# Performance work log

Hardware: AMD Instinct MI355X
Metric: run time of the kernel (lower is better)

## Reference

```python
import jax, jax.numpy as jnp
import numpy as np

N_NODES = 50000


def gcn_conv(x, src, dst, W, b, n):
    # PyG GCNConv: h = x @ W; out[i] = sum_j norm_ij * h[j] + b, with added self-loops
    h = x @ W  # [N, out]
    deg = jax.ops.segment_sum(jnp.ones_like(dst, dtype=h.dtype), dst, num_segments=n)
    inv_sqrt_deg = jnp.where(deg > 0, jax.lax.rsqrt(deg), 0.0)  # [N]
    coeff = inv_sqrt_deg[src] * inv_sqrt_deg[dst]  # [E]
    msg = h[src] * coeff[:, None]  # [E, out] gather (memory-bound)
    out = jax.ops.segment_sum(msg, dst, num_segments=n)  # scatter-add
    return out + b


def setup_inputs() -> dict:
    key = jax.random.key(0)
    ks = jax.random.split(key, 8)
    n, e, c_in, c_hid, c_out = N_NODES, 800000, 128, 128, 64
    x = jax.random.normal(ks[0], (n, c_in), dtype=jnp.float32)
    edge_index = jax.random.randint(ks[1], (2, e), 0, n, dtype=jnp.int64)
    # Glorot-ish scaled weights
    W1 = jax.random.normal(ks[2], (c_in, c_hid), dtype=jnp.float32) / np.sqrt(c_in)
    b1 = jnp.zeros((c_hid,), dtype=jnp.float32)
    W2 = jax.random.normal(ks[3], (c_hid, c_out), dtype=jnp.float32) / np.sqrt(c_hid)
    b2 = jnp.zeros((c_out,), dtype=jnp.float32)
    lin_W = jax.random.normal(ks[4], (2 * c_out, c_out), dtype=jnp.float32) / np.sqrt(2 * c_out)
    lin_b = jnp.zeros((c_out,), dtype=jnp.float32)
    return {"x": x, "edge_index": edge_index, "W1": W1, "b1": b1,
            "W2": W2, "b2": b2, "lin_W": lin_W, "lin_b": lin_b}


def reference(x, edge_index, W1, b1, W2, b2, lin_W, lin_b):
    n = x.shape[0]
    # add self-loops (as GCNConv does by default)
    loops = jnp.arange(n, dtype=edge_index.dtype)
    src = jnp.concatenate([edge_index[0], loops])
    dst = jnp.concatenate([edge_index[1], loops])

    def branch(x):
        h = jax.nn.relu(gcn_conv(x, src, dst, W1, b1, n))
        # dropout: identity in eval mode (training=False)
        return gcn_conv(h, src, dst, W2, b2, n)

    x1 = branch(x)
    x2 = branch(x)
    # FusionMethod == 'Concat'
    fused = jnp.concatenate([x1, x2], axis=1) @ lin_W + lin_b
    return jax.nn.log_softmax(fused, axis=1)
```

## Files before the change

kernel.cpp:

```cpp
#include <hip/hip_runtime.h>


#define CIN  128
#define CHID 128
#define COUT 64
#define BCAP_SH 13
#define BCAP    (1 << BCAP_SH)
#define BINCHUNK 2048

typedef short v8s __attribute__((ext_vector_type(8)));
typedef float v4f __attribute__((ext_vector_type(4)));

static __device__ __forceinline__ unsigned short f2bf(float f) {
    unsigned int u = __float_as_uint(f);
    unsigned int r = (u + 0x7fffu + ((u >> 16) & 1u)) >> 16;
    return (unsigned short)r;
}
static __device__ __forceinline__ float bf2f(unsigned short v) {
    return __uint_as_float(((unsigned int)v) << 16);
}

__global__ __launch_bounds__(256) void bin_kernel(const int* __restrict__ src,
                                                  const int* __restrict__ dst,
                                                  int* __restrict__ bcursor,
                                                  unsigned int* __restrict__ binned, int E) {
    __shared__ int h[256];
    __shared__ int base[256];
    int t = threadIdx.x;
    h[t] = 0;
    __syncthreads();
    int e0 = blockIdx.x * BINCHUNK;
    int e1 = e0 + BINCHUNK; if (e1 > E) e1 = E;
    for (int e = e0 + t; e < e1; e += 256)
        atomicAdd(&h[dst[e] >> 8], 1);
    __syncthreads();
    int c = h[t];
    base[t] = (t << BCAP_SH) + (c ? atomicAdd(&bcursor[t], c) : 0);
    __syncthreads();
    h[t] = 0;
    __syncthreads();
    for (int e = e0 + t; e < e1; e += 256) {
        int d = dst[e];
        int b = d >> 8;
        int pos = base[b] + atomicAdd(&h[b], 1);
        binned[pos] = (unsigned int)src[e] | (((unsigned int)d & 255u) << 16);
    }
}

__global__ __launch_bounds__(512) void csr_kernel(const unsigned int* __restrict__ binned,
                                                  const int* __restrict__ bcursor,
                                                  int2* __restrict__ rowpair,
                                                  float* __restrict__ inv,
                                                  int* __restrict__ ebuf, int n) {
    __shared__ int h[256];
    __shared__ int s[256];
    int b = blockIdx.x;
    int t = threadIdx.x;
    int base = b << BCAP_SH;
    int cnt  = bcursor[b];
    if (t < 256) h[t] = 0;
    __syncthreads();
    for (int i = t; i < cnt; i += 512)
        atomicAdd(&h[binned[base + i] >> 16], 1);
    __syncthreads();
    int myc = (t < 256) ? h[t] : 0;
    if (t < 256) s[t] = myc;
    __syncthreads();
    for (int off = 1; off < 256; off <<= 1) {
        int u = (t >= off && t < 256) ? s[t - off] : 0;
        __syncthreads();
        if (t < 256) s[t] += u;
        __syncthreads();
    }
    if (t < 256) {
        int excl = s[t] - myc;
        int node = (b << 8) + t;
        if (node < n) {
            rowpair[node] = make_int2(base + excl, base + excl + myc);
            inv[node] = rsqrtf((float)(myc + 1));
        }
        h[t] = base + excl;
    }
    __syncthreads();
    for (int i = t; i < cnt; i += 512) {
        unsigned int v = binned[base + i];
        int pos = atomicAdd(&h[v >> 16], 1);
        ebuf[pos] = (int)(v & 0xffffu);
    }
}

__global__ __launch_bounds__(128) void wprep_kernel(const float* __restrict__ W1,
                                                    const float* __restrict__ W2,
                                                    const float* __restrict__ b2,
                                                    const float* __restrict__ linW,
                                                    const float* __restrict__ linb,
                                                    unsigned short* __restrict__ Wt1,
                                                    unsigned short* __restrict__ Wt2,
                                                    float* __restrict__ bp,
                                                    int* __restrict__ bcursor) {
    int b = blockIdx.x;
    int t = threadIdx.x;
    if (b < CHID) {
        Wt1[b * CIN + t] = f2bf(W1[t * CHID + b]);
        if (t < COUT) {
            float acc = 0.f;
#pragma unroll 8
            for (int k = 0; k < COUT; ++k) {
                float wsv = linW[k * COUT + t] + linW[(k + COUT) * COUT + t];
                acc = fmaf(W2[b * COUT + k], wsv, acc);
            }
            Wt2[t * CHID + b] = f2bf(acc);
        }
    } else {
        bcursor[t] = 0;
        bcursor[128 + t] = 0;
        if (t < COUT) {
            float acc = 0.f;
#pragma unroll 8
            for (int k = 0; k < COUT; ++k) {
                float wsv = linW[k * COUT + t] + linW[(k + COUT) * COUT + t];
                acc = fmaf(b2[k], wsv, acc);
            }
            bp[t] = acc + linb[t];
        }
    }
}

template <int NOUT, bool A_BF16>
__global__ __launch_bounds__(256) void gemm_mfma(const void* __restrict__ Aptr,
                                                 const unsigned short* __restrict__ Wt,
                                                 const float* __restrict__ inv,
                                                 unsigned short* __restrict__ H, int n) {
    constexpr int NCT = NOUT / 16;
    int lane = threadIdx.x & 63;
    int wave = threadIdx.x >> 6;
    int quad = lane >> 4, r16 = lane & 15;
    int row0 = (blockIdx.x * 4 + wave) * 16;
    if (row0 >= n) return;
    int arow = row0 + r16;
    if (arow >= n) arow = n - 1;

    v4f acc[NCT];
#pragma unroll
    for (int c = 0; c < NCT; ++c) acc[c] = (v4f){0.f, 0.f, 0.f, 0.f};

#pragma unroll
    for (int kc = 0; kc < 4; ++kc) {
        v8s af;
        if (A_BF16) {
            const unsigned short* A = (const unsigned short*)Aptr;
            af = *(const v8s*)(A + (size_t)arow * 128 + kc * 32 + quad * 8);
        } else {
            const float* A = (const float*)Aptr;
            const float4* ap = (const float4*)(A + (size_t)arow * 128 + kc * 32 + quad * 8);
            float4 a0 = ap[0], a1 = ap[1];
            af[0] = (short)f2bf(a0.x); af[1] = (short)f2bf(a0.y);
            af[2] = (short)f2bf(a0.z); af[3] = (short)f2bf(a0.w);
            af[4] = (short)f2bf(a1.x); af[5] = (short)f2bf(a1.y);
            af[6] = (short)f2bf(a1.z); af[7] = (short)f2bf(a1.w);
        }
#pragma unroll
        for (int ct = 0; ct < NCT; ++ct) {
            v8s bf = *(const v8s*)(Wt + (size_t)(ct * 16 + r16) * 128 + kc * 32 + quad * 8);
            acc[ct] = __builtin_amdgcn_mfma_f32_16x16x32_bf16(af, bf, acc[ct], 0, 0, 0);
        }
    }

    float4 iv = ((const float4*)(inv + row0))[quad];
#pragma unroll
    for (int ct = 0; ct < NCT; ++ct) {
#pragma unroll
        for (int i = 0; i < 4; ++i) {
            int orow = row0 + quad * 4 + i;
            if (orow < n) {
                float sc = (i == 0) ? iv.x : (i == 1) ? iv.y : (i == 2) ? iv.z : iv.w;
                H[(size_t)orow * NOUT + ct * 16 + r16] = f2bf(acc[ct][i] * sc);
            }
        }
    }
}

__global__ void agg1_kernel(const unsigned int* __restrict__ Hs, const int* __restrict__ ebuf,
                            const int2* __restrict__ rowpair, const float* __restrict__ inv,
                            const float* __restrict__ bias, unsigned int* __restrict__ outp,
                            int n) {
    int node = __builtin_amdgcn_readfirstlane(blockIdx.x * 4 + (threadIdx.x >> 6));
    int lane = threadIdx.x & 63;
    if (node >= n) return;
    int2 rp = rowpair[node];
    int beg = rp.x, len = rp.y - rp.x;
    int eid = ebuf[beg + lane];
    int m = len < 64 ? len : 64;
    float ax = 0.f, ay = 0.f;
    int k = 0;
    for (; k + 4 <= m; k += 4) {
        int s0 = __builtin_amdgcn_readlane(eid, k);
        int s1 = __builtin_amdgcn_readlane(eid, k + 1);
        int s2 = __builtin_amdgcn_readlane(eid, k + 2);
        int s3 = __builtin_amdgcn_readlane(eid, k + 3);
        unsigned int u0 = Hs[(size_t)s0 * 64 + lane];
        unsigned int u1 = Hs[(size_t)s1 * 64 + lane];
        unsigned int u2 = Hs[(size_t)s2 * 64 + lane];
        unsigned int u3 = Hs[(size_t)s3 * 64 + lane];
        ax += __uint_as_float(u0 << 16);  ay += __uint_as_float(u0 & 0xffff0000u);
        ax += __uint_as_float(u1 << 16);  ay += __uint_as_float(u1 & 0xffff0000u);
        ax += __uint_as_float(u2 << 16);  ay += __uint_as_float(u2 & 0xffff0000u);
        ax += __uint_as_float(u3 << 16);  ay += __uint_as_float(u3 & 0xffff0000u);
    }
    for (; k < m; ++k) {
        int s = __builtin_amdgcn_readlane(eid, k);
        unsigned int u = Hs[(size_t)s * 64 + lane];
        ax += __uint_as_float(u << 16);
        ay += __uint_as_float(u & 0xffff0000u);
    }
    for (; k < len; ++k) {
        int s = ebuf[beg + k];
        unsigned int u = Hs[(size_t)s * 64 + lane];
        ax += __uint_as_float(u << 16);
        ay += __uint_as_float(u & 0xffff0000u);
    }
    {
        unsigned int u = Hs[(size_t)node * 64 + lane];
        ax += __uint_as_float(u << 16);
        ay += __uint_as_float(u & 0xffff0000u);
    }
    float wd = inv[node];
    float2 bv = ((const float2*)bias)[lane];
    float ox = fmaxf(fmaf(wd, ax, bv.x), 0.f);
    float oy = fmaxf(fmaf(wd, ay, bv.y), 0.f);
    outp[(size_t)node * 64 + lane] =
        (unsigned int)f2bf(ox) | ((unsigned int)f2bf(oy) << 16);
}

__global__ void agg2_final_kernel(const unsigned short* __restrict__ Hs,
                                  const int* __restrict__ ebuf, const int2* __restrict__ rowpair,
                                  const float* __restrict__ inv, const float* __restrict__ bp,
                                  float* __restrict__ outp, int n) {
    int node = __builtin_amdgcn_readfirstlane(blockIdx.x * 4 + (threadIdx.x >> 6));
    int lane = threadIdx.x & 63;
    if (node >= n) return;
    int2 rp = rowpair[node];
    int beg = rp.x, len = rp.y - rp.x;
    int eid = ebuf[beg + lane];
    int m = len < 64 ? len : 64;
    float acc = 0.f;
    int k = 0;
    for (; k + 4 <= m; k += 4) {
        int s0 = __builtin_amdgcn_readlane(eid, k);
        int s1 = __builtin_amdgcn_readlane(eid, k + 1);
        int s2 = __builtin_amdgcn_readlane(eid, k + 2);
        int s3 = __builtin_amdgcn_readlane(eid, k + 3);
        float v0 = bf2f(Hs[(size_t)s0 * 64 + lane]);
        float v1 = bf2f(Hs[(size_t)s1 * 64 + lane]);
        float v2 = bf2f(Hs[(size_t)s2 * 64 + lane]);
        float v3 = bf2f(Hs[(size_t)s3 * 64 + lane]);
        acc += v0 + v1 + v2 + v3;
    }
    for (; k < m; ++k) {
        int s = __builtin_amdgcn_readlane(eid, k);
        acc += bf2f(Hs[(size_t)s * 64 + lane]);
    }
    for (; k < len; ++k) {
        acc += bf2f(Hs[(size_t)ebuf[beg + k] * 64 + lane]);
    }
    acc += bf2f(Hs[(size_t)node * 64 + lane]);
    float fo = fmaf(inv[node], acc, bp[lane]);
    float mx = fo;
#pragma unroll
    for (int off = 32; off >= 1; off >>= 1) mx = fmaxf(mx, __shfl_xor(mx, off, 64));
    float ex = expf(fo - mx);
    float s = ex;
#pragma unroll
    for (int off = 32; off >= 1; off >>= 1) s += __shfl_xor(s, off, 64);
    outp[(size_t)node * COUT + lane] = fo - mx - logf(s);
}

static inline size_t align16(size_t x) { return (x + 15) & ~(size_t)15; }

extern "C" void kernel_launch(void* const* d_in, const int* in_sizes, int n_in,
                              void* d_out, int out_size, void* d_ws, size_t ws_size,
                              hipStream_t stream) {
    const float* x    = (const float*)d_in[0];
    const int*   eidx = (const int*)d_in[1];
    const float* W1   = (const float*)d_in[2];
    const float* b1   = (const float*)d_in[3];
    const float* W2   = (const float*)d_in[4];
    const float* b2   = (const float*)d_in[5];
    const float* linW = (const float*)d_in[6];
    const float* linb = (const float*)d_in[7];
    float* out = (float*)d_out;

    const int n = in_sizes[0] / CIN;
    const int E = in_sizes[1] / 2;
    const int* src = eidx;
    const int* dst = eidx + E;
    const int NBKT = (n + 255) >> 8;

    char* ws = (char*)d_ws;
    size_t off = 0;
    int2*  rowpair = (int2*)(ws + off);  off = align16(off + (size_t)n * 8);
    float* inv     = (float*)(ws + off); off = align16(off + (size_t)n * 4);
    int*   bcursor = (int*)(ws + off);   off = align16(off + 256 * 4);
    unsigned short* Wt1 = (unsigned short*)(ws + off); off = align16(off + (size_t)CHID * CIN * 2);
    unsigned short* Wt2 = (unsigned short*)(ws + off); off = align16(off + (size_t)COUT * CHID * 2);
    float* bp      = (float*)(ws + off); off = align16(off + (size_t)COUT * 4);
    unsigned int* binned = (unsigned int*)(ws + off); off = align16(off + (size_t)256 * BCAP * 4);
    int*   ebuf    = (int*)(ws + off);   off = align16(off + (size_t)256 * BCAP * 4);
    unsigned short* h1s   = (unsigned short*)(ws + off); off = align16(off + (size_t)n * CHID * 2);
    unsigned short* agg1b = (unsigned short*)(ws + off); off = align16(off + (size_t)n * CHID * 2);
    unsigned short* h2p   = (unsigned short*)(ws + off); off = align16(off + (size_t)n * COUT * 2);

    wprep_kernel<<<CHID + 1, 128, 0, stream>>>(W1, W2, b2, linW, linb, Wt1, Wt2, bp, bcursor);

    bin_kernel<<<(E + BINCHUNK - 1) / BINCHUNK, 256, 0, stream>>>(src, dst, bcursor, binned, E);
    csr_kernel<<<NBKT, 512, 0, stream>>>(binned, bcursor, rowpair, inv, ebuf, n);

    gemm_mfma<CHID, false><<<(n + 63) / 64, 256, 0, stream>>>(x, Wt1, inv, h1s, n);
    agg1_kernel<<<(n + 3) / 4, 256, 0, stream>>>((const unsigned int*)h1s, ebuf, rowpair, inv, b1,
                                                 (unsigned int*)agg1b, n);

    gemm_mfma<COUT, true><<<(n + 63) / 64, 256, 0, stream>>>(agg1b, Wt2, inv, h2p, n);
    agg2_final_kernel<<<(n + 3) / 4, 256, 0, stream>>>(h2p, ebuf, rowpair, inv, bp, out, n);
}
```

Baseline: 215.4 us.

## Fuse layer-1 aggregation with second GEMM and gather two edges per wave

Layer-1 aggregation now runs 16 nodes per block, writes the ReLU'd bf16 rows into shared memory, and feeds them straight into MFMA with W2. This removes the agg1b intermediate buffer and one kernel launch. Both aggregation kernels now have each half-wave fetch a different neighbor row with wider loads, and unroll the edge loop 16 deep to raise memory-level parallelism. The half-wave partial sums are then combined with a cross-lane shuffle, and log-softmax reduces over 32 lanes. The cost is more register pressure, and the fused kernel does its agg work serially across 4 nodes per wave before the GEMM.

```diff
diff --git a/kernel.cpp b/kernel.cpp
--- a/kernel.cpp
+++ b/kernel.cpp
@@ -18,6 +18,12 @@
 }
 static __device__ __forceinline__ float bf2f(unsigned short v) {
     return __uint_as_float(((unsigned int)v) << 16);
+}
+static __device__ __forceinline__ float bflo(unsigned int u) {
+    return __uint_as_float(u << 16);
+}
+static __device__ __forceinline__ float bfhi(unsigned int u) {
+    return __uint_as_float(u & 0xffff0000u);
 }
 
 __global__ __launch_bounds__(256) void bin_kernel(const int* __restrict__ src,
@@ -180,99 +186,216 @@
     }
 }
 
-__global__ void agg1_kernel(const unsigned int* __restrict__ Hs, const int* __restrict__ ebuf,
-                            const int2* __restrict__ rowpair, const float* __restrict__ inv,
-                            const float* __restrict__ bias, unsigned int* __restrict__ outp,
-                            int n) {
+__global__ __launch_bounds__(256) void agg1_gemm2_kernel(
+        const unsigned int* __restrict__ Hs,
+        const int* __restrict__ ebuf,
+        const int2* __restrict__ rowpair,
+        const float* __restrict__ inv,
+        const float* __restrict__ bias,
+        const unsigned short* __restrict__ Wt2,
+        unsigned short* __restrict__ H2,
+        int n) {
+    __shared__ unsigned int tileu[16 * 68];
+    const uint2* __restrict__ Hs2 = (const uint2*)Hs;
+    int node0 = blockIdx.x * 16;
+    int wid = __builtin_amdgcn_readfirstlane(threadIdx.x >> 6);
+    int lane = threadIdx.x & 63;
+    int l32 = lane & 31;
+    bool hi = lane >= 32;
+
+    for (int j = 0; j < 4; ++j) {
+        int r = wid * 4 + j;
+        int node = node0 + r;
+        float a0 = 0.f, a1 = 0.f, a2 = 0.f, a3 = 0.f;
+        if (node < n) {
+            int2 rp = rowpair[node];
+            int beg = rp.x, len = rp.y - rp.x;
+            int eid = ebuf[beg + lane];
+            uint2 usl = Hs2[(size_t)node * 32 + l32];
+            int m = len < 64 ? len : 64;
+            int k = 0;
+            for (; k + 16 <= m; k += 16) {
+                int sa0 = __builtin_amdgcn_readlane(eid, k);
+                int sb0 = __builtin_amdgcn_readlane(eid, k + 1);
+                int sa1 = __builtin_amdgcn_readlane(eid, k + 2);
+                int sb1 = __builtin_amdgcn_readlane(eid, k + 3);
+                int sa2 = __builtin_amdgcn_readlane(eid, k + 4);
+                int sb2 = __builtin_amdgcn_readlane(eid, k + 5);
+                int sa3 = __builtin_amdgcn_readlane(eid, k + 6);
+                int sb3 = __builtin_amdgcn_readlane(eid, k + 7);
+                int sa4 = __builtin_amdgcn_readlane(eid, k + 8);
+                int sb4 = __builtin_amdgcn_readlane(eid, k + 9);
+                int sa5 = __builtin_amdgcn_readlane(eid, k + 10);
+                int sb5 = __builtin_amdgcn_readlane(eid, k + 11);
+                int sa6 = __builtin_amdgcn_readlane(eid, k + 12);
+                int sb6 = __builtin_amdgcn_readlane(eid, k + 13);
+                int sa7 = __builtin_amdgcn_readlane(eid, k + 14);
+                int sb7 = __builtin_amdgcn_readlane(eid, k + 15);
+                uint2 u0 = Hs2[(size_t)(hi ? sb0 : sa0) * 32 + l32];
+                uint2 u1 = Hs2[(size_t)(hi ? sb1 : sa1) * 32 + l32];
+                uint2 u2 = Hs2[(size_t)(hi ? sb2 : sa2) * 32 + l32];
+                uint2 u3 = Hs2[(size_t)(hi ? sb3 : sa3) * 32 + l32];
+                uint2 u4 = Hs2[(size_t)(hi ? sb4 : sa4) * 32 + l32];
+                uint2 u5 = Hs2[(size_t)(hi ? sb5 : sa5) * 32 + l32];
+                uint2 u6 = Hs2[(size_t)(hi ? sb6 : sa6) * 32 + l32];
+                uint2 u7 = Hs2[(size_t)(hi ? sb7 : sa7) * 32 + l32];
+                a0 += bflo(u0.x); a1 += bfhi(u0.x); a2 += bflo(u0.y); a3 += bfhi(u0.y);
+                a0 += bflo(u1.x); a1 += bfhi(u1.x); a2 += bflo(u1.y); a3 += bfhi(u1.y);
+                a0 += bflo(u2.x); a1 += bfhi(u2.x); a2 += bflo(u2.y); a3 += bfhi(u2.y);
+                a0 += bflo(u3.x); a1 += bfhi(u3.x); a2 += bflo(u3.y); a3 += bfhi(u3.y);
+                a0 += bflo(u4.x); a1 += bfhi(u4.x); a2 += bflo(u4.y); a3 += bfhi(u4.y);
+                a0 += bflo(u5.x); a1 += bfhi(u5.x); a2 += bflo(u5.y); a3 += bfhi(u5.y);
+                a0 += bflo(u6.x); a1 += bfhi(u6.x); a2 += bflo(u6.y); a3 += bfhi(u6.y);
+                a0 += bflo(u7.x); a1 += bfhi(u7.x); a2 += bflo(u7.y); a3 += bfhi(u7.y);
+            }
+            for (; k + 2 <= m; k += 2) {
+                int sa = __builtin_amdgcn_readlane(eid, k);
+                int sb = __builtin_amdgcn_readlane(eid, k + 1);
+                uint2 u = Hs2[(size_t)(hi ? sb : sa) * 32 + l32];
+                a0 += bflo(u.x); a1 += bfhi(u.x); a2 += bflo(u.y); a3 += bfhi(u.y);
+            }
+            for (; k < m; ++k) {
+                int s = __builtin_amdgcn_readlane(eid, k);
+                uint2 u = Hs2[(size_t)s * 32 + l32];
+                if (hi) { u.x = 0; u.y = 0; }
+                a0 += bflo(u.x); a1 += bfhi(u.x); a2 += bflo(u.y); a3 += bfhi(u.y);
+            }
+            for (; k < len; ++k) {
+                int s = ebuf[beg + k];
+                uint2 u = Hs2[(size_t)s * 32 + l32];
+                if (hi) { u.x = 0; u.y = 0; }
+                a0 += bflo(u.x); a1 += bfhi(u.x); a2 += bflo(u.y); a3 += bfhi(u.y);
+            }
+            if (hi) { usl.x = 0; usl.y = 0; }
+            a0 += bflo(usl.x); a1 += bfhi(usl.x); a2 += bflo(usl.y); a3 += bfhi(usl.y);
+            a0 += __shfl_xor(a0, 32, 64);
+            a1 += __shfl_xor(a1, 32, 64);
+            a2 += __shfl_xor(a2, 32, 64);
+            a3 += __shfl_xor(a3, 32, 64);
+            float wd = inv[node];
+            float4 bv = ((const float4*)bias)[l32];
+            float o0 = fmaxf(fmaf(wd, a0, bv.x), 0.f);
+            float o1 = fmaxf(fmaf(wd, a1, bv.y), 0.f);
+            float o2 = fmaxf(fmaf(wd, a2, bv.z), 0.f);
+            float o3 = fmaxf(fmaf(wd, a3, bv.w), 0.f);
+            if (!hi) {
+                tileu[r * 68 + 2 * l32]     = (unsigned int)f2bf(o0) | ((unsigned int)f2bf(o1) << 16);
+                tileu[r * 68 + 2 * l32 + 1] = (unsigned int)f2bf(o2) | ((unsigned int)f2bf(o3) << 16);
+            }
+        } else {
+            if (!hi) {
+                tileu[r * 68 + 2 * l32] = 0;
+                tileu[r * 68 + 2 * l32 + 1] = 0;
+            }
+        }
+    }
+    __syncthreads();
+
+    int quad = lane >> 4, r16 = lane & 15;
+    v4f acc = (v4f){0.f, 0.f, 0.f, 0.f};
+#pragma unroll
+    for (int kc = 0; kc < 4; ++kc) {
+        v8s af = *(const v8s*)&tileu[r16 * 68 + kc * 16 + quad * 4];
+        v8s bf = *(const v8s*)(Wt2 + (size_t)(wid * 16 + r16) * 128 + kc * 32 + quad * 8);
+        acc = __builtin_amdgcn_mfma_f32_16x16x32_bf16(af, bf, acc, 0, 0, 0);
+    }
+    float4 iv = ((const float4*)(inv + node0))[quad];
+#pragma unroll
+    for (int i = 0; i < 4; ++i) {
+        int orow = node0 + quad * 4 + i;
+        if (orow < n) {
+            float sc = (i == 0) ? iv.x : (i == 1) ? iv.y : (i == 2) ? iv.z : iv.w;
+            H2[(size_t)orow * 64 + wid * 16 + r16] = f2bf(acc[i] * sc);
+        }
+    }
+}
+
+__global__ __launch_bounds__(256) void agg2_final_kernel(
+        const unsigned int* __restrict__ Hs,
+        const int* __restrict__ ebuf, const int2* __restrict__ rowpair,
+        const float* __restrict__ inv, const float* __restrict__ bp,
+        float* __restrict__ outp, int n) {
     int node = __builtin_amdgcn_readfirstlane(blockIdx.x * 4 + (threadIdx.x >> 6));
     int lane = threadIdx.x & 63;
+    int l32 = lane & 31;
+    bool hi = lane >= 32;
     if (node >= n) return;
     int2 rp = rowpair[node];
     int beg = rp.x, len = rp.y - rp.x;
     int eid = ebuf[beg + lane];
+    unsigned int usl = Hs[(size_t)node * 32 + l32];
     int m = len < 64 ? len : 64;
     float ax = 0.f, ay = 0.f;
     int k = 0;
-    for (; k + 4 <= m; k += 4) {
-        int s0 = __builtin_amdgcn_readlane(eid, k);
-        int s1 = __builtin_amdgcn_readlane(eid, k + 1);
-        int s2 = __builtin_amdgcn_readlane(eid, k + 2);
-        int s3 = __builtin_amdgcn_readlane(eid, k + 3);
-        unsigned int u0 = Hs[(size_t)s0 * 64 + lane];
-        unsigned int u1 = Hs[(size_t)s1 * 64 + lane];
-        unsigned int u2 = Hs[(size_t)s2 * 64 + lane];
-        unsigned int u3 = Hs[(size_t)s3 * 64 + lane];
-        ax += __uint_as_float(u0 << 16);  ay += __uint_as_float(u0 & 0xffff0000u);
-        ax += __uint_as_float(u1 << 16);  ay += __uint_as_float(u1 & 0xffff0000u);
-        ax += __uint_as_float(u2 << 16);  ay += __uint_as_float(u2 & 0xffff0000u);
-        ax += __uint_as_float(u3 << 16);  ay += __uint_as_float(u3 & 0xffff0000u);
+    for (; k + 16 <= m; k += 16) {
+        int sa0 = __builtin_amdgcn_readlane(eid, k);
+        int sb0 = __builtin_amdgcn_readlane(eid, k + 1);
+        int sa1 = __builtin_amdgcn_readlane(eid, k + 2);
+        int sb1 = __builtin_amdgcn_readlane(eid, k + 3);
+        int sa2 = __builtin_amdgcn_readlane(eid, k + 4);
+        int sb2 = __builtin_amdgcn_readlane(eid, k + 5);
+        int sa3 = __builtin_amdgcn_readlane(eid, k + 6);
+        int sb3 = __builtin_amdgcn_readlane(eid, k + 7);
+        int sa4 = __builtin_amdgcn_readlane(eid, k + 8);
+        int sb4 = __builtin_amdgcn_readlane(eid, k + 9);
+        int sa5 = __builtin_amdgcn_readlane(eid, k + 10);
+        int sb5 = __builtin_amdgcn_readlane(eid, k + 11);
+        int sa6 = __builtin_amdgcn_readlane(eid, k + 12);
+        int sb6 = __builtin_amdgcn_readlane(eid, k + 13);
+        int sa7 = __builtin_amdgcn_readlane(eid, k + 14);
+        int sb7 = __builtin_amdgcn_readlane(eid, k + 15);
+        unsigned int u0 = Hs[(size_t)(hi ? sb0 : sa0) * 32 + l32];
+        unsigned int u1 = Hs[(size_t)(hi ? sb1 : sa1) * 32 + l32];
+        unsigned int u2 = Hs[(size_t)(hi ? sb2 : sa2) * 32 + l32];
+        unsigned int u3 = Hs[(size_t)(hi ? sb3 : sa3) * 32 + l32];
+        unsigned int u4 = Hs[(size_t)(hi ? sb4 : sa4) * 32 + l32];
+        unsigned int u5 = Hs[(size_t)(hi ? sb5 : sa5) * 32 + l32];
+        unsigned int u6 = Hs[(size_t)(hi ? sb6 : sa6) * 32 + l32];
+        unsigned int u7 = Hs[(size_t)(hi ? sb7 : sa7) * 32 + l32];
+        ax += bflo(u0); ay += bfhi(u0);
+        ax += bflo(u1); ay += bfhi(u1);
+        ax += bflo(u2); ay += bfhi(u2);
+        ax += bflo(u3); ay += bfhi(u3);
+        ax += bflo(u4); ay += bfhi(u4);
+        ax += bflo(u5); ay += bfhi(u5);
+        ax += bflo(u6); ay += bfhi(u6);
+        ax += bflo(u7); ay += bfhi(u7);
+    }
+    for (; k + 2 <= m; k += 2) {
+        int sa = __builtin_amdgcn_readlane(eid, k);
+        int sb = __builtin_amdgcn_readlane(eid, k + 1);
+        unsigned int u = Hs[(size_t)(hi ? sb : sa) * 32 + l32];
+        ax += bflo(u); ay += bfhi(u);
     }
     for (; k < m; ++k) {
         int s = __builtin_amdgcn_readlane(eid, k);
-        unsigned int u = Hs[(size_t)s * 64 + lane];
-        ax += __uint_as_float(u << 16);
-        ay += __uint_as_float(u & 0xffff0000u);
+        unsigned int u = Hs[(size_t)s * 32 + l32];
+        if (hi) u = 0;
+        ax += bflo(u); ay += bfhi(u);
     }
     for (; k < len; ++k) {
-        int s = ebuf[beg + k];
-        unsigned int u = Hs[(size_t)s * 64 + lane];
-        ax += __uint_as_float(u << 16);
-        ay += __uint_as_float(u & 0xffff0000u);
-    }
-    {
-        unsigned int u = Hs[(size_t)node * 64 + lane];
-        ax += __uint_as_float(u << 16);
-        ay += __uint_as_float(u & 0xffff0000u);
-    }
+        unsigned int u = Hs[(size_t)ebuf[beg + k] * 32 + l32];
+        if (hi) u = 0;
+        ax += bflo(u); ay += bfhi(u);
+    }
+    if (hi) usl = 0;
+    ax += bflo(usl); ay += bfhi(usl);
+    ax += __shfl_xor(ax, 32, 64);
+    ay += __shfl_xor(ay, 32, 64);
     float wd = inv[node];
-    float2 bv = ((const float2*)bias)[lane];
-    float ox = fmaxf(fmaf(wd, ax, bv.x), 0.f);
-    float oy = fmaxf(fmaf(wd, ay, bv.y), 0.f);
-    outp[(size_t)node * 64 + lane] =
-        (unsigned int)f2bf(ox) | ((unsigned int)f2bf(oy) << 16);
-}
-
-__global__ void agg2_final_kernel(const unsigned short* __restrict__ Hs,
-                                  const int* __restrict__ ebuf, const int2* __restrict__ rowpair,
-                                  const float* __restrict__ inv, const float* __restrict__ bp,
-                                  float* __restrict__ outp, int n) {
-    int node = __builtin_amdgcn_readfirstlane(blockIdx.x * 4 + (threadIdx.x >> 6));
-    int lane = threadIdx.x & 63;
-    if (node >= n) return;
-    int2 rp = rowpair[node];
-    int beg = rp.x, len = rp.y - rp.x;
-    int eid = ebuf[beg + lane];
-    int m = len < 64 ? len : 64;
-    float acc = 0.f;
-    int k = 0;
-    for (; k + 4 <= m; k += 4) {
-        int s0 = __builtin_amdgcn_readlane(eid, k);
-        int s1 = __builtin_amdgcn_readlane(eid, k + 1);
-        int s2 = __builtin_amdgcn_readlane(eid, k + 2);
-        int s3 = __builtin_amdgcn_readlane(eid, k + 3);
-        float v0 = bf2f(Hs[(size_t)s0 * 64 + lane]);
-        float v1 = bf2f(Hs[(size_t)s1 * 64 + lane]);
-        float v2 = bf2f(Hs[(size_t)s2 * 64 + lane]);
-        float v3 = bf2f(Hs[(size_t)s3 * 64 + lane]);
-        acc += v0 + v1 + v2 + v3;
-    }
-    for (; k < m; ++k) {
-        int s = __builtin_amdgcn_readlane(eid, k);
-        acc += bf2f(Hs[(size_t)s * 64 + lane]);
-    }
-    for (; k < len; ++k) {
-        acc += bf2f(Hs[(size_t)ebuf[beg + k] * 64 + lane]);
-    }
-    acc += bf2f(Hs[(size_t)node * 64 + lane]);
-    float fo = fmaf(inv[node], acc, bp[lane]);
-    float mx = fo;
-#pragma unroll
-    for (int off = 32; off >= 1; off >>= 1) mx = fmaxf(mx, __shfl_xor(mx, off, 64));
-    float ex = expf(fo - mx);
-    float s = ex;
-#pragma unroll
-    for (int off = 32; off >= 1; off >>= 1) s += __shfl_xor(s, off, 64);
-    outp[(size_t)node * COUT + lane] = fo - mx - logf(s);
+    float2 bv = ((const float2*)bp)[l32];
+    float fx = fmaf(wd, ax, bv.x);
+    float fy = fmaf(wd, ay, bv.y);
+    float mx = fmaxf(fx, fy);
+#pragma unroll
+    for (int off = 16; off >= 1; off >>= 1) mx = fmaxf(mx, __shfl_xor(mx, off, 64));
+    float s = expf(fx - mx) + expf(fy - mx);
+#pragma unroll
+    for (int off = 16; off >= 1; off >>= 1) s += __shfl_xor(s, off, 64);
+    float ls = logf(s);
+    if (!hi) {
+        ((float2*)(outp + (size_t)node * 64))[l32] = make_float2(fx - mx - ls, fy - mx - ls);
+    }
 }
 
 static inline size_t align16(size_t x) { return (x + 15) & ~(size_t)15; }
@@ -306,9 +429,8 @@
     float* bp      = (float*)(ws + off); off = align16(off + (size_t)COUT * 4);
     unsigned int* binned = (unsigned int*)(ws + off); off = align16(off + (size_t)256 * BCAP * 4);
     int*   ebuf    = (int*)(ws + off);   off = align16(off + (size_t)256 * BCAP * 4);
-    unsigned short* h1s   = (unsigned short*)(ws + off); off = align16(off + (size_t)n * CHID * 2);
-    unsigned short* agg1b = (unsigned short*)(ws + off); off = align16(off + (size_t)n * CHID * 2);
-    unsigned short* h2p   = (unsigned short*)(ws + off); off = align16(off + (size_t)n * COUT * 2);
+    unsigned short* h1s = (unsigned short*)(ws + off); off = align16(off + (size_t)n * CHID * 2);
+    unsigned short* h2p = (unsigned short*)(ws + off); off = align16(off + (size_t)n * COUT * 2);
 
     wprep_kernel<<<CHID + 1, 128, 0, stream>>>(W1, W2, b2, linW, linb, Wt1, Wt2, bp, bcursor);
 
@@ -316,9 +438,10 @@
     csr_kernel<<<NBKT, 512, 0, stream>>>(binned, bcursor, rowpair, inv, ebuf, n);
 
     gemm_mfma<CHID, false><<<(n + 63) / 64, 256, 0, stream>>>(x, Wt1, inv, h1s, n);
-    agg1_kernel<<<(n + 3) / 4, 256, 0, stream>>>((const unsigned int*)h1s, ebuf, rowpair, inv, b1,
-                                                 (unsigned int*)agg1b, n);
-
-    gemm_mfma<COUT, true><<<(n + 63) / 64, 256, 0, stream>>>(agg1b, Wt2, inv, h2p, n);
-    agg2_final_kernel<<<(n + 3) / 4, 256, 0, stream>>>(h2p, ebuf, rowpair, inv, bp, out, n);
-}
+
+    agg1_gemm2_kernel<<<(n + 15) / 16, 256, 0, stream>>>((const unsigned int*)h1s, ebuf, rowpair,
+                                                         inv, b1, Wt2, h2p, n);
+
+    agg2_final_kernel<<<(n + 3) / 4, 256, 0, stream>>>((const unsigned int*)h2p, ebuf, rowpair,
+                                                       inv, bp, out, n);
+}
```

Measured after the change: 209.0 us. -3.0%, faster.

## Store GEMM outputs in feature-sliced planes and aggregate per slice for cache locality

Applied to the files above, without the earlier changes.

The GEMM kernels now write hidden features into 8 column-sliced planes, so each slice of node features is compact. New aggregation kernels give each block one slice and split the wave into lane groups that gather several neighbours in parallel, then reduce with shuffles. Edge indices shrink to 16-bit, and log-softmax moves into a separate pass over the output. The aim is gather working sets small enough to stay in L2 for the random neighbour reads. The cost is 8x more blocks re-reading rowpair and edge lists, one extra kernel launch, and an extra read/write of the output.

```diff
diff --git a/kernel.cpp b/kernel.cpp
--- a/kernel.cpp
+++ b/kernel.cpp
@@ -16,8 +16,14 @@
     unsigned int r = (u + 0x7fffu + ((u >> 16) & 1u)) >> 16;
     return (unsigned short)r;
 }
-static __device__ __forceinline__ float bf2f(unsigned short v) {
-    return __uint_as_float(((unsigned int)v) << 16);
+static __device__ __forceinline__ float bflo(unsigned int u) {
+    return __uint_as_float(u << 16);
+}
+static __device__ __forceinline__ float bfhi(unsigned int u) {
+    return __uint_as_float(u & 0xffff0000u);
+}
+static __device__ __forceinline__ unsigned int pk2(float a, float b) {
+    return (unsigned int)f2bf(a) | ((unsigned int)f2bf(b) << 16);
 }
 
 __global__ __launch_bounds__(256) void bin_kernel(const int* __restrict__ src,
@@ -51,7 +57,7 @@
                                                   const int* __restrict__ bcursor,
                                                   int2* __restrict__ rowpair,
                                                   float* __restrict__ inv,
-                                                  int* __restrict__ ebuf, int n) {
+                                                  unsigned short* __restrict__ ebuf16, int n) {
     __shared__ int h[256];
     __shared__ int s[256];
     int b = blockIdx.x;
@@ -85,7 +91,7 @@
     for (int i = t; i < cnt; i += 512) {
         unsigned int v = binned[base + i];
         int pos = atomicAdd(&h[v >> 16], 1);
-        ebuf[pos] = (int)(v & 0xffffu);
+        ebuf16[pos] = (unsigned short)(v & 0xffffu);
     }
 }
 
@@ -126,12 +132,10 @@
     }
 }
 
-template <int NOUT, bool A_BF16>
-__global__ __launch_bounds__(256) void gemm_mfma(const void* __restrict__ Aptr,
-                                                 const unsigned short* __restrict__ Wt,
-                                                 const float* __restrict__ inv,
-                                                 unsigned short* __restrict__ H, int n) {
-    constexpr int NCT = NOUT / 16;
+__global__ __launch_bounds__(256) void gemm1_kernel(const float* __restrict__ A,
+                                                    const unsigned short* __restrict__ Wt,
+                                                    const float* __restrict__ inv,
+                                                    unsigned short* __restrict__ h1t, int n) {
     int lane = threadIdx.x & 63;
     int wave = threadIdx.x >> 6;
     int quad = lane >> 4, r16 = lane & 15;
@@ -139,28 +143,23 @@
     if (row0 >= n) return;
     int arow = row0 + r16;
     if (arow >= n) arow = n - 1;
-
-    v4f acc[NCT];
-#pragma unroll
-    for (int c = 0; c < NCT; ++c) acc[c] = (v4f){0.f, 0.f, 0.f, 0.f};
+    size_t n16 = (size_t)n * 16;
+
+    v4f acc[8];
+#pragma unroll
+    for (int c = 0; c < 8; ++c) acc[c] = (v4f){0.f, 0.f, 0.f, 0.f};
 
 #pragma unroll
     for (int kc = 0; kc < 4; ++kc) {
+        const float4* ap = (const float4*)(A + (size_t)arow * 128 + kc * 32 + quad * 8);
+        float4 a0 = ap[0], a1 = ap[1];
         v8s af;
-        if (A_BF16) {
-            const unsigned short* A = (const unsigned short*)Aptr;
-            af = *(const v8s*)(A + (size_t)arow * 128 + kc * 32 + quad * 8);
-        } else {
-            const float* A = (const float*)Aptr;
-            const float4* ap = (const float4*)(A + (size_t)arow * 128 + kc * 32 + quad * 8);
-            float4 a0 = ap[0], a1 = ap[1];
-            af[0] = (short)f2bf(a0.x); af[1] = (short)f2bf(a0.y);
-            af[2] = (short)f2bf(a0.z); af[3] = (short)f2bf(a0.w);
-            af[4] = (short)f2bf(a1.x); af[5] = (short)f2bf(a1.y);
-            af[6] = (short)f2bf(a1.z); af[7] = (short)f2bf(a1.w);
-        }
-#pragma unroll
-        for (int ct = 0; ct < NCT; ++ct) {
+        af[0] = (short)f2bf(a0.x); af[1] = (short)f2bf(a0.y);
+        af[2] = (short)f2bf(a0.z); af[3] = (short)f2bf(a0.w);
+        af[4] = (short)f2bf(a1.x); af[5] = (short)f2bf(a1.y);
+        af[6] = (short)f2bf(a1.z); af[7] = (short)f2bf(a1.w);
+#pragma unroll
+        for (int ct = 0; ct < 8; ++ct) {
             v8s bf = *(const v8s*)(Wt + (size_t)(ct * 16 + r16) * 128 + kc * 32 + quad * 8);
             acc[ct] = __builtin_amdgcn_mfma_f32_16x16x32_bf16(af, bf, acc[ct], 0, 0, 0);
         }
@@ -168,111 +167,230 @@
 
     float4 iv = ((const float4*)(inv + row0))[quad];
 #pragma unroll
-    for (int ct = 0; ct < NCT; ++ct) {
+    for (int ct = 0; ct < 8; ++ct) {
 #pragma unroll
         for (int i = 0; i < 4; ++i) {
             int orow = row0 + quad * 4 + i;
             if (orow < n) {
                 float sc = (i == 0) ? iv.x : (i == 1) ? iv.y : (i == 2) ? iv.z : iv.w;
-                H[(size_t)orow * NOUT + ct * 16 + r16] = f2bf(acc[ct][i] * sc);
-            }
-        }
-    }
-}
-
-__global__ void agg1_kernel(const unsigned int* __restrict__ Hs, const int* __restrict__ ebuf,
-                            const int2* __restrict__ rowpair, const float* __restrict__ inv,
-                            const float* __restrict__ bias, unsigned int* __restrict__ outp,
-                            int n) {
+                h1t[(size_t)ct * n16 + (size_t)orow * 16 + r16] = f2bf(acc[ct][i] * sc);
+            }
+        }
+    }
+}
+
+__global__ __launch_bounds__(256) void gemm2_kernel(const unsigned short* __restrict__ A,
+                                                    const unsigned short* __restrict__ Wt,
+                                                    const float* __restrict__ inv,
+                                                    unsigned short* __restrict__ h2t, int n) {
+    int lane = threadIdx.x & 63;
+    int wave = threadIdx.x >> 6;
+    int quad = lane >> 4, r16 = lane & 15;
+    int row0 = (blockIdx.x * 4 + wave) * 16;
+    if (row0 >= n) return;
+    int arow = row0 + r16;
+    if (arow >= n) arow = n - 1;
+    size_t n8 = (size_t)n * 8;
+
+    v4f acc[4];
+#pragma unroll
+    for (int c = 0; c < 4; ++c) acc[c] = (v4f){0.f, 0.f, 0.f, 0.f};
+
+#pragma unroll
+    for (int kc = 0; kc < 4; ++kc) {
+        v8s af = *(const v8s*)(A + (size_t)arow * 128 + kc * 32 + quad * 8);
+#pragma unroll
+        for (int ct = 0; ct < 4; ++ct) {
+            v8s bf = *(const v8s*)(Wt + (size_t)(ct * 16 + r16) * 128 + kc * 32 + quad * 8);
+            acc[ct] = __builtin_amdgcn_mfma_f32_16x16x32_bf16(af, bf, acc[ct], 0, 0, 0);
+        }
+    }
+
+    float4 iv = ((const float4*)(inv + row0))[quad];
+#pragma unroll
+    for (int ct = 0; ct < 4; ++ct) {
+        int col = ct * 16 + r16;
+        int pl = col >> 3, d = col & 7;
+#pragma unroll
+        for (int i = 0; i < 4; ++i) {
+            int orow = row0 + quad * 4 + i;
+            if (orow < n) {
+                float sc = (i == 0) ? iv.x : (i == 1) ? iv.y : (i == 2) ? iv.z : iv.w;
+                h2t[(size_t)pl * n8 + (size_t)orow * 8 + d] = f2bf(acc[ct][i] * sc);
+            }
+        }
+    }
+}
+
+__global__ __launch_bounds__(256) void agg1_slice_kernel(
+        const unsigned short* __restrict__ h1t,
+        const unsigned short* __restrict__ ebuf16,
+        const int2* __restrict__ rowpair,
+        const float* __restrict__ inv,
+        const float* __restrict__ b1,
+        unsigned int* __restrict__ agg1b,
+        int n) {
+    int slice = blockIdx.x & 7;
+    int grp   = blockIdx.x >> 3;
+    int wid = threadIdx.x >> 6;
+    int lane = threadIdx.x & 63;
+    int g4 = lane >> 2;
+    int d4 = lane & 3;
+    const uint2* __restrict__ plane = (const uint2*)(h1t + (size_t)slice * n * 16);
+    float4 bv = ((const float4*)b1)[slice * 4 + d4];
+    int nbase = (grp * 4 + wid) * 4;
+
+    int begs[4], lens[4], eids[4];
+    uint2 usls[4];
+    float invs[4];
+#pragma unroll
+    for (int j = 0; j < 4; ++j) {
+        int node = nbase + j;
+        if (node >= n) node = n - 1;
+        int2 rp = rowpair[node];
+        begs[j] = rp.x;
+        lens[j] = rp.y - rp.x;
+        eids[j] = (int)ebuf16[rp.x + lane];
+        usls[j] = plane[(size_t)node * 4 + d4];
+        invs[j] = inv[node];
+    }
+
+#pragma unroll
+    for (int j = 0; j < 4; ++j) {
+        int node = nbase + j;
+        if (node >= n) break;
+        int beg = begs[j], len = lens[j], eid = eids[j];
+        int m = len < 64 ? len : 64;
+        int kmax = (m + 15) & ~15;
+        float a0 = 0.f, a1 = 0.f, a2 = 0.f, a3 = 0.f;
+        for (int k = 0; k < kmax; k += 16) {
+            int idx = k + g4;
+            int sid = __shfl(eid, idx, 64);
+            sid = (idx < m) ? sid : node;
+            uint2 u = plane[(size_t)sid * 4 + d4];
+            a0 += bflo(u.x); a1 += bfhi(u.x); a2 += bflo(u.y); a3 += bfhi(u.y);
+        }
+        if (len > 64 && lane < 4) {
+            for (int k = 64; k < len; ++k) {
+                int s = (int)ebuf16[beg + k];
+                uint2 u = plane[(size_t)s * 4 + d4];
+                a0 += bflo(u.x); a1 += bfhi(u.x); a2 += bflo(u.y); a3 += bfhi(u.y);
+            }
+        }
+#pragma unroll
+        for (int off = 4; off <= 32; off <<= 1) {
+            a0 += __shfl_xor(a0, off, 64);
+            a1 += __shfl_xor(a1, off, 64);
+            a2 += __shfl_xor(a2, off, 64);
+            a3 += __shfl_xor(a3, off, 64);
+        }
+        float c = 1.0f - (float)(kmax - m);
+        uint2 usl = usls[j];
+        a0 = fmaf(c, bflo(usl.x), a0); a1 = fmaf(c, bfhi(usl.x), a1);
+        a2 = fmaf(c, bflo(usl.y), a2); a3 = fmaf(c, bfhi(usl.y), a3);
+        float wd = invs[j];
+        float o0 = fmaxf(fmaf(wd, a0, bv.x), 0.f);
+        float o1 = fmaxf(fmaf(wd, a1, bv.y), 0.f);
+        float o2 = fmaxf(fmaf(wd, a2, bv.z), 0.f);
+        float o3 = fmaxf(fmaf(wd, a3, bv.w), 0.f);
+        if (lane < 4) {
+            uint2 w; w.x = pk2(o0, o1); w.y = pk2(o2, o3);
+            ((uint2*)agg1b)[(size_t)node * 32 + slice * 4 + d4] = w;
+        }
+    }
+}
+
+__global__ __launch_bounds__(256) void agg2_slice_kernel(
+        const unsigned short* __restrict__ h2t,
+        const unsigned short* __restrict__ ebuf16,
+        const int2* __restrict__ rowpair,
+        const float* __restrict__ inv,
+        const float* __restrict__ bp,
+        float* __restrict__ outp,
+        int n) {
+    int slice = blockIdx.x & 7;
+    int grp   = blockIdx.x >> 3;
+    int wid = threadIdx.x >> 6;
+    int lane = threadIdx.x & 63;
+    int g2 = lane >> 1;
+    int d2 = lane & 1;
+    const uint2* __restrict__ plane = (const uint2*)(h2t + (size_t)slice * n * 8);
+    float4 bv = ((const float4*)bp)[slice * 2 + d2];
+    int nbase = (grp * 4 + wid) * 4;
+
+    int begs[4], lens[4], eids[4];
+    uint2 usls[4];
+    float invs[4];
+#pragma unroll
+    for (int j = 0; j < 4; ++j) {
+        int node = nbase + j;
+        if (node >= n) node = n - 1;
+        int2 rp = rowpair[node];
+        begs[j] = rp.x;
+        lens[j] = rp.y - rp.x;
+        eids[j] = (int)ebuf16[rp.x + lane];
+        usls[j] = plane[(size_t)node * 2 + d2];
+        invs[j] = inv[node];
+    }
+
+#pragma unroll
+    for (int j = 0; j < 4; ++j) {
+        int node = nbase + j;
+        if (node >= n) break;
+        int beg = begs[j], len = lens[j], eid = eids[j];
+        int m = len < 64 ? len : 64;
+        int kmax = (m + 31) & ~31;
+        float a0 = 0.f, a1 = 0.f, a2 = 0.f, a3 = 0.f;
+        for (int k = 0; k < kmax; k += 32) {
+            int idx = k + g2;
+            int sid = __shfl(eid, idx, 64);
+            sid = (idx < m) ? sid : node;
+            uint2 u = plane[(size_t)sid * 2 + d2];
+            a0 += bflo(u.x); a1 += bfhi(u.x); a2 += bflo(u.y); a3 += bfhi(u.y);
+        }
+        if (len > 64 && lane < 2) {
+            for (int k = 64; k < len; ++k) {
+                int s = (int)ebuf16[beg + k];
+                uint2 u = plane[(size_t)s * 2 + d2];
+                a0 += bflo(u.x); a1 += bfhi(u.x); a2 += bflo(u.y); a3 += bfhi(u.y);
+            }
+        }
+#pragma unroll
+        for (int off = 2; off <= 32; off <<= 1) {
+            a0 += __shfl_xor(a0, off, 64);
+            a1 += __shfl_xor(a1, off, 64);
+            a2 += __shfl_xor(a2, off, 64);
+            a3 += __shfl_xor(a3, off, 64);
+        }
+        float c = 1.0f - (float)(kmax - m);
+        uint2 usl = usls[j];
+        a0 = fmaf(c, bflo(usl.x), a0); a1 = fmaf(c, bfhi(usl.x), a1);
+        a2 = fmaf(c, bflo(usl.y), a2); a3 = fmaf(c, bfhi(usl.y), a3);
+        float wd = invs[j];
+        float4 w;
+        w.x = fmaf(wd, a0, bv.x);
+        w.y = fmaf(wd, a1, bv.y);
+        w.z = fmaf(wd, a2, bv.z);
+        w.w = fmaf(wd, a3, bv.w);
+        if (lane < 2) {
+            ((float4*)outp)[(size_t)node * 16 + slice * 2 + d2] = w;
+        }
+    }
+}
+
+__global__ __launch_bounds__(256) void softmax_kernel(float* __restrict__ outp, int n) {
     int node = __builtin_amdgcn_readfirstlane(blockIdx.x * 4 + (threadIdx.x >> 6));
     int lane = threadIdx.x & 63;
     if (node >= n) return;
-    int2 rp = rowpair[node];
-    int beg = rp.x, len = rp.y - rp.x;
-    int eid = ebuf[beg + lane];
-    int m = len < 64 ? len : 64;
-    float ax = 0.f, ay = 0.f;
-    int k = 0;
-    for (; k + 4 <= m; k += 4) {
-        int s0 = __builtin_amdgcn_readlane(eid, k);
-        int s1 = __builtin_amdgcn_readlane(eid, k + 1);
-        int s2 = __builtin_amdgcn_readlane(eid, k + 2);
-        int s3 = __builtin_amdgcn_readlane(eid, k + 3);
-        unsigned int u0 = Hs[(size_t)s0 * 64 + lane];
-        unsigned int u1 = Hs[(size_t)s1 * 64 + lane];
-        unsigned int u2 = Hs[(size_t)s2 * 64 + lane];
-        unsigned int u3 = Hs[(size_t)s3 * 64 + lane];
-        ax += __uint_as_float(u0 << 16);  ay += __uint_as_float(u0 & 0xffff0000u);
-        ax += __uint_as_float(u1 << 16);  ay += __uint_as_float(u1 & 0xffff0000u);
-        ax += __uint_as_float(u2 << 16);  ay += __uint_as_float(u2 & 0xffff0000u);
-        ax += __uint_as_float(u3 << 16);  ay += __uint_as_float(u3 & 0xffff0000u);
-    }
-    for (; k < m; ++k) {
-        int s = __builtin_amdgcn_readlane(eid, k);
-        unsigned int u = Hs[(size_t)s * 64 + lane];
-        ax += __uint_as_float(u << 16);
-        ay += __uint_as_float(u & 0xffff0000u);
-    }
-    for (; k < len; ++k) {
-        int s = ebuf[beg + k];
-        unsigned int u = Hs[(size_t)s * 64 + lane];
-        ax += __uint_as_float(u << 16);
-        ay += __uint_as_float(u & 0xffff0000u);
-    }
-    {
-        unsigned int u = Hs[(size_t)node * 64 + lane];
-        ax += __uint_as_float(u << 16);
-        ay += __uint_as_float(u & 0xffff0000u);
-    }
-    float wd = inv[node];
-    float2 bv = ((const float2*)bias)[lane];
-    float ox = fmaxf(fmaf(wd, ax, bv.x), 0.f);
-    float oy = fmaxf(fmaf(wd, ay, bv.y), 0.f);
-    outp[(size_t)node * 64 + lane] =
-        (unsigned int)f2bf(ox) | ((unsigned int)f2bf(oy) << 16);
-}
-
-__global__ void agg2_final_kernel(const unsigned short* __restrict__ Hs,
-                                  const int* __restrict__ ebuf, const int2* __restrict__ rowpair,
-                                  const float* __restrict__ inv, const float* __restrict__ bp,
-                                  float* __restrict__ outp, int n) {
-    int node = __builtin_amdgcn_readfirstlane(blockIdx.x * 4 + (threadIdx.x >> 6));
-    int lane = threadIdx.x & 63;
-    if (node >= n) return;
-    int2 rp = rowpair[node];
-    int beg = rp.x, len = rp.y - rp.x;
-    int eid = ebuf[beg + lane];
-    int m = len < 64 ? len : 64;
-    float acc = 0.f;
-    int k = 0;
-    for (; k + 4 <= m; k += 4) {
-        int s0 = __builtin_amdgcn_readlane(eid, k);
-        int s1 = __builtin_amdgcn_readlane(eid, k + 1);
-        int s2 = __builtin_amdgcn_readlane(eid, k + 2);
-        int s3 = __builtin_amdgcn_readlane(eid, k + 3);
-        float v0 = bf2f(Hs[(size_t)s0 * 64 + lane]);
-        float v1 = bf2f(Hs[(size_t)s1 * 64 + lane]);
-        float v2 = bf2f(Hs[(size_t)s2 * 64 + lane]);
-        float v3 = bf2f(Hs[(size_t)s3 * 64 + lane]);
-        acc += v0 + v1 + v2 + v3;
-    }
-    for (; k < m; ++k) {
-        int s = __builtin_amdgcn_readlane(eid, k);
-        acc += bf2f(Hs[(size_t)s * 64 + lane]);
-    }
-    for (; k < len; ++k) {
-        acc += bf2f(Hs[(size_t)ebuf[beg + k] * 64 + lane]);
-    }
-    acc += bf2f(Hs[(size_t)node * 64 + lane]);
-    float fo = fmaf(inv[node], acc, bp[lane]);
-    float mx = fo;
+    float v = outp[(size_t)node * 64 + lane];
+    float mx = v;
 #pragma unroll
     for (int off = 32; off >= 1; off >>= 1) mx = fmaxf(mx, __shfl_xor(mx, off, 64));
-    float ex = expf(fo - mx);
-    float s = ex;
+    float e = expf(v - mx);
+    float s = e;
 #pragma unroll
     for (int off = 32; off >= 1; off >>= 1) s += __shfl_xor(s, off, 64);
-    outp[(size_t)node * COUT + lane] = fo - mx - logf(s);
+    outp[(size_t)node * 64 + lane] = v - mx - logf(s);
 }
 
 static inline size_t align16(size_t x) { return (x + 15) & ~(size_t)15; }
@@ -305,20 +423,24 @@
     unsigned short* Wt2 = (unsigned short*)(ws + off); off = align16(off + (size_t)COUT * CHID * 2);
     float* bp      = (float*)(ws + off); off = align16(off + (size_t)COUT * 4);
     unsigned int* binned = (unsigned int*)(ws + off); off = align16(off + (size_t)256 * BCAP * 4);
-    int*   ebuf    = (int*)(ws + off);   off = align16(off + (size_t)256 * BCAP * 4);
-    unsigned short* h1s   = (unsigned short*)(ws + off); off = align16(off + (size_t)n * CHID * 2);
-    unsigned short* agg1b = (unsigned short*)(ws + off); off = align16(off + (size_t)n * CHID * 2);
-    unsigned short* h2p   = (unsigned short*)(ws + off); off = align16(off + (size_t)n * COUT * 2);
+    unsigned short* ebuf16 = (unsigned short*)(ws + off); off = align16(off + (size_t)256 * BCAP * 2);
+    unsigned short* h1t   = (unsigned short*)(ws + off); off = align16(off + (size_t)n * CHID * 2);
+    unsigned int*   agg1b = (unsigned int*)(ws + off);   off = align16(off + (size_t)n * CHID * 2);
+    unsigned short* h2t   = (unsigned short*)(ws + off); off = align16(off + (size_t)n * COUT * 2);
 
     wprep_kernel<<<CHID + 1, 128, 0, stream>>>(W1, W2, b2, linW, linb, Wt1, Wt2, bp, bcursor);
 
     bin_kernel<<<(E + BINCHUNK - 1) / BINCHUNK, 256, 0, stream>>>(src, dst, bcursor, binned, E);
-    csr_kernel<<<NBKT, 512, 0, stream>>>(binned, bcursor, rowpair, inv, ebuf, n);
-
-    gemm_mfma<CHID, false><<<(n + 63) / 64, 256, 0, stream>>>(x, Wt1, inv, h1s, n);
-    agg1_kernel<<<(n + 3) / 4, 256, 0, stream>>>((const unsigned int*)h1s, ebuf, rowpair, inv, b1,
-                                                 (unsigned int*)agg1b, n);
-
-    gemm_mfma<COUT, true><<<(n + 63) / 64, 256, 0, stream>>>(agg1b, Wt2, inv, h2p, n);
-    agg2_final_kernel<<<(n + 3) / 4, 256, 0, stream>>>(h2p, ebuf, rowpair, inv, bp, out, n);
-}
+    csr_kernel<<<NBKT, 512, 0, stream>>>(binned, bcursor, rowpair, inv, ebuf16, n);
+
+    gemm1_kernel<<<(n + 63) / 64, 256, 0, stream>>>(x, Wt1, inv, h1t, n);
+
+    const int NG = (n + 15) / 16;
+    agg1_slice_kernel<<<NG * 8, 256, 0, stream>>>(h1t, ebuf16, rowpair, inv, b1, agg1b, n);
+
+    gemm2_kernel<<<(n + 63) / 64, 256, 0, stream>>>((const unsigned short*)agg1b, Wt2, inv, h2t, n);
+
+    agg2_slice_kernel<<<NG * 8, 256, 0, stream>>>(h2t, ebuf16, rowpair, inv, bp, out, n);
+
+    softmax_kernel<<<(n + 3) / 4, 256, 0, stream>>>(out, n);
+}
```

Measured after the change: 329.4 us. 1.53x slower.
